# Optimization experiments

Hardware: AMD Instinct MI355X
Metric: run time of the kernel (lower is better)

Reference implementation:

```python
import jax, jax.numpy as jnp
import numpy as np
from jax import lax

EPS_IN = 1e-5  # torch InstanceNorm1d eps


def instance_norm(x, w, b):
    # x: (B, C, T); normalize over T per (B, C), biased variance
    mu = x.mean(axis=-1, keepdims=True)
    var = x.var(axis=-1, keepdims=True)
    return (x - mu) * lax.rsqrt(var + EPS_IN) * w[None, :, None] + b[None, :, None]


def conv1x1(x, w):
    # w: (O, I, 1)
    return jnp.einsum('oi,bit->bot', w[:, :, 0], x)


def setup_inputs() -> dict:
    key = jax.random.key(0)
    ks = jax.random.split(key, 16)
    B, C, T, NC = 32, 64, 2048, 4
    enc_dim = C * 3 * 4
    d = {
        'xb': jax.random.normal(ks[0], (B, 3, C, T), jnp.float32),
        'mu': jnp.linspace(-3.0, 3.0, 4),
        'sigma': jnp.full((4,), 2.0),
        'sconv1_w': jax.random.normal(ks[1], (128, enc_dim, 1)) * (1.0 / np.sqrt(enc_dim)),
        'in1_w': 1.0 + 0.1 * jax.random.normal(ks[2], (128,)),
        'in1_b': 0.1 * jax.random.normal(ks[3], (128,)),
        'sconv2_w': jax.random.normal(ks[4], (C, 128, 1)) * (1.0 / np.sqrt(128)),
        'in2_w': 1.0 + 0.1 * jax.random.normal(ks[5], (C,)),
        'in2_b': 0.1 * jax.random.normal(ks[6], (C,)),
        'tconv1_w': jax.random.normal(ks[7], (C, C, 15)) * (1.0 / np.sqrt(C * 15)),
        'in3_w': 1.0 + 0.1 * jax.random.normal(ks[8], (C,)),
        'in3_b': 0.1 * jax.random.normal(ks[9], (C,)),
        'tconv2_w': jax.random.normal(ks[10], (C, C, 1)) * (1.0 / np.sqrt(C)),
        'in4_w': 1.0 + 0.1 * jax.random.normal(ks[11], (C,)),
        'in4_b': 0.1 * jax.random.normal(ks[12], (C,)),
        'alpha': jnp.asarray(0.5),
        'gamma': jnp.asarray(0.5),
        'beta_logit': jnp.asarray(1.0),
        'fc_w': jax.random.normal(ks[13], (4, C)) * (1.0 / np.sqrt(C)),
        'fc_b': 0.1 * jax.random.normal(ks[14], (4,)),
    }
    return d


def reference(xb, mu, sigma, sconv1_w, in1_w, in1_b, sconv2_w, in2_w, in2_b,
              tconv1_w, in3_w, in3_b, tconv2_w, in4_w, in4_b,
              alpha, gamma, beta_logit, fc_w, fc_b):
    B, Ftypes, C, T = xb.shape
    V_BASE = 1.0
    Tp = T // 8

    # pooled curvature / tangent streams -> (T', B, C)
    curv_p = xb[:, 1].reshape(B, C, Tp, 8).mean(-1).transpose(2, 0, 1)
    tang_p = xb[:, 2].reshape(B, C, Tp, 8).mean(-1).transpose(2, 0, 1)

    # learnable population encoding: (B,3,C,T,4) -> (B, 3*C*4, T)
    enc = jnp.exp(-(xb[..., None] - mu) ** 2 / (2.0 * sigma ** 2 + 1e-6))
    x_enc = enc.transpose(0, 1, 2, 4, 3).reshape(B, Ftypes * C * 4, T)

    # spatial 1x1 convs + instance norm + relu
    h = jax.nn.relu(instance_norm(conv1x1(x_enc, sconv1_w), in1_w, in1_b))
    h = jax.nn.relu(instance_norm(conv1x1(h, sconv2_w), in2_w, in2_b))

    # temporal conv k=15 pad=7, 1x1 conv, avg pool 8
    h = lax.conv_general_dilated(h, tconv1_w, (1,), [(7, 7)],
                                 dimension_numbers=('NCH', 'OIH', 'NCH'))
    h = jax.nn.relu(instance_norm(h, in3_w, in3_b))
    h = jax.nn.relu(instance_norm(conv1x1(h, tconv2_w), in4_w, in4_b))
    h = h.reshape(B, C, Tp, 8).mean(-1)  # AvgPool1d(8)
    # dropout is identity in eval mode
    c = h.transpose(2, 0, 1)  # (T', B, C)

    # sequential GD-LIF recurrence over T' steps
    def step(m, inp):
        x_t, curv_t, tang_t = inp
        v_th = V_BASE + alpha * tang_t
        beta = jax.nn.sigmoid(beta_logit - gamma * curv_t)
        m_next = beta * m + x_t
        spike = (m_next - v_th > 0).astype(m_next.dtype)
        m_next = m_next - spike * v_th
        return m_next, spike

    m0 = jnp.zeros((B, C), xb.dtype)
    _, spikes = lax.scan(step, m0, (c, curv_p, tang_p))  # (T', B, C)

    attn = jax.nn.softmax(curv_p, axis=0)
    out_feat = jnp.sum(spikes * attn, axis=0)  # (B, C)
    return out_feat @ fc_w.T + fc_b
```

## Files before the change

### kernel.cpp

```cpp
#include <hip/hip_runtime.h>
#include <math.h>

#define TLEN 2048
#define TP 256

typedef double d4 __attribute__((ext_vector_type(4)));

__device__ __forceinline__ double block_reduce_sum_d(double v, double* sm) {
#pragma unroll
  for (int off = 32; off > 0; off >>= 1) v += __shfl_down(v, off, 64);
  int lane = threadIdx.x & 63, wid = threadIdx.x >> 6;
  __syncthreads();
  if (lane == 0) sm[wid] = v;
  __syncthreads();
  double r = sm[0] + sm[1] + sm[2] + sm[3];
  __syncthreads();
  return r;
}

__global__ void k_probe_f64(int* __restrict__ tbl) {
  int l = threadIdx.x;
  __shared__ int kaS[64], kbS[64];
  __shared__ int cnt[256];
  int rdv[4] = {-1, -1, -1, -1}, cdv[4] = {-1, -1, -1, -1};
  int mav = -1, nbv = -1;
  int okr = 1;
  int nrow = 0, ncol = 0;
  kaS[l] = -1; kbS[l] = -1;
  __syncthreads();

  for (int j = 0; j < 64; ++j) {
    double a = (l == j) ? 1.0 : 0.0;
    d4 acc = {0.0, 0.0, 0.0, 0.0};
    acc = __builtin_amdgcn_mfma_f64_16x16x4f64(a, 1.0, acc, 0, 0, 0);
    int mylab = -1;
#pragma unroll
    for (int v = 0; v < 4; ++v) if (acc[v] != 0.0 && rdv[v] >= 0) mylab = rdv[v];
#pragma unroll
    for (int off = 32; off >= 1; off >>= 1) {
      int o = __shfl_xor(mylab, off);
      mylab = mylab > o ? mylab : o;
    }
    int label = (mylab < 0) ? nrow : mylab;
    if (mylab < 0) nrow++;
    if (label >= 16) okr = 0;
#pragma unroll
    for (int v = 0; v < 4; ++v) if (acc[v] != 0.0) rdv[v] = label;
    if (l == j) mav = label;
  }

  for (int j = 0; j < 64; ++j) {
    double bb = (l == j) ? 1.0 : 0.0;
    d4 acc = {0.0, 0.0, 0.0, 0.0};
    acc = __builtin_amdgcn_mfma_f64_16x16x4f64(1.0, bb, acc, 0, 0, 0);
    int mylab = -1;
#pragma unroll
    for (int v = 0; v < 4; ++v) if (acc[v] != 0.0 && cdv[v] >= 0) mylab = cdv[v];
#pragma unroll
    for (int off = 32; off >= 1; off >>= 1) {
      int o = __shfl_xor(mylab, off);
      mylab = mylab > o ? mylab : o;
    }
    int label = (mylab < 0) ? ncol : mylab;
    if (mylab < 0) ncol++;
    if (label >= 16) okr = 0;
#pragma unroll
    for (int v = 0; v < 4; ++v) if (acc[v] != 0.0) cdv[v] = label;
    if (l == j) nbv = label;
  }

  unsigned long long row0 = __ballot(mav == 0);
  if (__popcll(row0) != 4) okr = 0;
  for (int i = 0; i < 4; ++i) {
    int rep = -1, idx = -1;
    for (int t = 0; t < 64; ++t)
      if ((row0 >> t) & 1ull) { if (++idx == i) { rep = t; break; } }
    double a = (l == rep) ? 1.0 : 0.0;
    double bb = (double)(l + 1);
    d4 acc = {0.0, 0.0, 0.0, 0.0};
    acc = __builtin_amdgcn_mfma_f64_16x16x4f64(a, bb, acc, 0, 0, 0);
#pragma unroll
    for (int v = 0; v < 4; ++v)
      if (rdv[v] == 0) {
        int jp = (int)(acc[v] + 0.5) - 1;
        if (jp >= 0 && jp < 64) kbS[jp] = i; else okr = 0;
      }
  }
  __syncthreads();
  int kbv = kbS[l];

  for (int i = 0; i < 4; ++i) {
    unsigned long long bm = __ballot(kbv == i);
    int rep = -1;
    if (bm != 0ull) { rep = 0; while (!((bm >> rep) & 1ull)) ++rep; }
    else okr = 0;
    int nc = (rep >= 0) ? __shfl(nbv, rep) : -2;
    double bb = (l == rep) ? 1.0 : 0.0;
    double aa = (double)(l + 1);
    d4 acc = {0.0, 0.0, 0.0, 0.0};
    acc = __builtin_amdgcn_mfma_f64_16x16x4f64(aa, bb, acc, 0, 0, 0);
#pragma unroll
    for (int v = 0; v < 4; ++v)
      if (cdv[v] == nc) {
        int jp = (int)(acc[v] + 0.5) - 1;
        if (jp >= 0 && jp < 64) kaS[jp] = i; else okr = 0;
      }
  }
  __syncthreads();
  int kav = kaS[l];

  if (nrow != 16 || ncol != 16) okr = 0;
  if (mav < 0 || mav > 15 || nbv < 0 || nbv > 15 ||
      kav < 0 || kav > 3 || kbv < 0 || kbv > 3) okr = 0;
#pragma unroll
  for (int v = 0; v < 4; ++v)
    if (rdv[v] < 0 || rdv[v] > 15 || cdv[v] < 0 || cdv[v] > 15) okr = 0;
  cnt[l] = 0; cnt[64 + l] = 0; cnt[128 + l] = 0; cnt[192 + l] = 0;
  __syncthreads();
  if (mav >= 0 && mav < 16 && kav >= 0 && kav < 4) atomicAdd(&cnt[mav * 4 + kav], 1);
  if (kbv >= 0 && kbv < 4 && nbv >= 0 && nbv < 16) atomicAdd(&cnt[64 + kbv * 16 + nbv], 1);
  __syncthreads();
  if (cnt[l] != 1 || cnt[64 + l] != 1) okr = 0;
  __syncthreads();
  cnt[l] = 0; cnt[64 + l] = 0; cnt[128 + l] = 0; cnt[192 + l] = 0;
  __syncthreads();
#pragma unroll
  for (int v = 0; v < 4; ++v)
    if (rdv[v] >= 0 && rdv[v] < 16 && cdv[v] >= 0 && cdv[v] < 16)
      atomicAdd(&cnt[rdv[v] * 16 + cdv[v]], 1);
  __syncthreads();
#pragma unroll
  for (int v = 0; v < 4; ++v) if (cnt[l * 4 + v] != 1) okr = 0;
  if (mav == 0) {
    int rank = (int)__popcll(row0 & ((1ull << l) - 1ull));
    if (kav != rank) okr = 0;
  }
  unsigned long long good = __ballot(okr != 0);
  tbl[l] = mav; tbl[64 + l] = kav; tbl[128 + l] = kbv; tbl[192 + l] = nbv;
#pragma unroll
  for (int v = 0; v < 4; ++v) {
    tbl[256 + l * 4 + v] = rdv[v];
    tbl[512 + l * 4 + v] = cdv[v];
  }
  if (l == 0) tbl[768] = (good == 0xFFFFFFFFFFFFFFFFull) ? 1 : 0;
}

__global__ void k_repack_w(const float* __restrict__ w, float* __restrict__ wT) {
  int idx = blockIdx.x * 256 + threadIdx.x;
  if (idx >= 64 * 64 * 15) return;
  int o = idx & 63, i = (idx >> 6) & 63, k = idx >> 12;
  wT[idx] = w[(o * 64 + i) * 15 + k];
}

template <typename T>
__global__ __launch_bounds__(256) void k_pool_ct(const float* __restrict__ xb,
                                                 T* __restrict__ curvp,
                                                 T* __restrict__ tangp) {
  int row = blockIdx.x;
  int b = row >> 6, c = row & 63;
  int tid = threadIdx.x;
  const float* s1 = xb + ((size_t)((b * 3 + 1) * 64 + c)) * TLEN + tid * 8;
  const float* s2 = xb + ((size_t)((b * 3 + 2) * 64 + c)) * TLEN + tid * 8;
  double p1 = 0.0, p2 = 0.0;
#pragma unroll
  for (int j = 0; j < 8; ++j) { p1 += (double)s1[j]; p2 += (double)s2[j]; }
  curvp[(size_t)row * TP + tid] = (T)(p1 * 0.125);
  tangp[(size_t)row * TP + tid] = (T)(p2 * 0.125);
}

template <typename T>
__global__ __launch_bounds__(256) void k_stats(const T* __restrict__ h,
                                               const float* __restrict__ gw,
                                               const float* __restrict__ gb,
                                               int chmask,
                                               double* __restrict__ sc,
                                               double* __restrict__ sh) {
  __shared__ double sm[4];
  int row = blockIdx.x, tid = threadIdx.x;
  int ch = row & chmask;
  const T* base = h + (size_t)row * TLEN + tid * 8;
  double v[8];
#pragma unroll
  for (int j = 0; j < 8; ++j) v[j] = (double)base[j];
  double s = 0.0;
#pragma unroll
  for (int j = 0; j < 8; ++j) s += v[j];
  double mean = block_reduce_sum_d(s, sm) * (1.0 / 2048.0);
  double sq = 0.0;
#pragma unroll
  for (int j = 0; j < 8; ++j) { double d = v[j] - mean; sq += d * d; }
  double var = block_reduce_sum_d(sq, sm) * (1.0 / 2048.0);
  double scale = (double)gw[ch] / sqrt(var + 1e-5);
  double shift = (double)gb[ch] - mean * scale;
  if (tid == 0) { sc[row] = scale; sh[row] = shift; }
}

template <typename T>
__global__ __launch_bounds__(256, 4) void k_enc1_mfma(const float* __restrict__ xb,
                                                      const float* __restrict__ w,
                                                      const float* __restrict__ mu,
                                                      const float* __restrict__ sigma,
                                                      T* __restrict__ h1,
                                                      const int* __restrict__ tbl) {
  if (tbl[768] == 0) return;
  __shared__ float AsT[32][132];
  __shared__ double Bs[32][68];
  __shared__ double smu[4], sinv[4];
  int b = blockIdx.x, t0 = blockIdx.y * 64, tid = threadIdx.x;
  int wv = tid >> 6, l = tid & 63;
  int t_ma = tbl[l], t_ka = tbl[64 + l], t_kb = tbl[128 + l], t_nb = tbl[192 + l];
  int t_rd[4], t_cd[4];
#pragma unroll
  for (int v = 0; v < 4; ++v) { t_rd[v] = tbl[256 + l * 4 + v]; t_cd[v] = tbl[512 + l * 4 + v]; }
  if (tid < 4) {
    smu[tid] = (double)mu[tid];
    double s = (double)sigma[tid];
    sinv[tid] = 1.0 / (2.0 * s * s + 1e-6);
  }
  d4 acc[2][4];
#pragma unroll
  for (int r = 0; r < 2; ++r)
#pragma unroll
    for (int c = 0; c < 4; ++c) acc[r][c] = (d4){0.0, 0.0, 0.0, 0.0};

  for (int kc = 0; kc < 24; ++kc) {
    int i0 = kc * 32;
    __syncthreads();
    {
      int idx = tid * 4;
#pragma unroll
      for (int rep = 0; rep < 4; ++rep) {
        int o = idx >> 5, ii = idx & 31;
        float4 v4 = *(const float4*)(w + (size_t)o * 768 + i0 + ii);
        AsT[ii][o] = v4.x; AsT[ii + 1][o] = v4.y; AsT[ii + 2][o] = v4.z; AsT[ii + 3][o] = v4.w;
        idx += 1024;
      }
    }
    {
      int f = i0 >> 8;
      int cb = (i0 >> 2) & 63;
      int c = tid >> 5, l2 = tid & 31;
      int t = 2 * l2;
      float2 x2 = *(const float2*)(xb + ((size_t)((b * 3 + f) * 64 + cb + c)) * TLEN + t0 + t);
      double xv0 = (double)x2.x, xv1 = (double)x2.y;
#pragma unroll
      for (int g = 0; g < 4; ++g) {
        double m = smu[g], inv = sinv[g];
        double d0 = xv0 - m, d1 = xv1 - m;
        double2 e = {exp(-d0 * d0 * inv), exp(-d1 * d1 * inv)};
        *(double2*)&Bs[c * 4 + g][t] = e;
      }
    }
    __syncthreads();
#pragma unroll
    for (int k4 = 0; k4 < 32; k4 += 4) {
      double aF0 = (double)AsT[k4 + t_ka][wv * 32 + t_ma];
      double aF1 = (double)AsT[k4 + t_ka][wv * 32 + 16 + t_ma];
      double bF[4];
#pragma unroll
      for (int c = 0; c < 4; ++c) bF[c] = Bs[k4 + t_kb][c * 16 + t_nb];
#pragma unroll
      for (int c = 0; c < 4; ++c) {
        acc[0][c] = __builtin_amdgcn_mfma_f64_16x16x4f64(aF0, bF[c], acc[0][c], 0, 0, 0);
        acc[1][c] = __builtin_amdgcn_mfma_f64_16x16x4f64(aF1, bF[c], acc[1][c], 0, 0, 0);
      }
    }
  }
#pragma unroll
  for (int r = 0; r < 2; ++r)
#pragma unroll
    for (int c = 0; c < 4; ++c)
#pragma unroll
      for (int v = 0; v < 4; ++v) {
        int o = wv * 32 + r * 16 + t_rd[v];
        h1[((size_t)(b * 128 + o)) * TLEN + t0 + c * 16 + t_cd[v]] = (T)acc[r][c][v];
      }
}

template <typename T>
__global__ __launch_bounds__(256, 4) void k_enc1_valu(const float* __restrict__ xb,
                                                      const float* __restrict__ w,
                                                      const float* __restrict__ mu,
                                                      const float* __restrict__ sigma,
                                                      T* __restrict__ h1,
                                                      const int* __restrict__ tbl) {
  if (tbl[768] != 0) return;
  __shared__ float AsT[32][132];
  __shared__ double Bs[32][64];
  __shared__ double smu[4], sinv[4];
  int b = blockIdx.x, t0 = blockIdx.y * 64, tid = threadIdx.x;
  if (tid < 4) {
    smu[tid] = (double)mu[tid];
    double s = (double)sigma[tid];
    sinv[tid] = 1.0 / (2.0 * s * s + 1e-6);
  }
  double acc[8][4] = {};
  int to = (tid >> 4) * 8, l = tid & 15;
  for (int kc = 0; kc < 24; ++kc) {
    int i0 = kc * 32;
    __syncthreads();
    {
      int idx = tid * 4;
#pragma unroll
      for (int rep = 0; rep < 4; ++rep) {
        int o = idx >> 5, ii = idx & 31;
        float4 v4 = *(const float4*)(w + (size_t)o * 768 + i0 + ii);
        AsT[ii][o] = v4.x; AsT[ii + 1][o] = v4.y; AsT[ii + 2][o] = v4.z; AsT[ii + 3][o] = v4.w;
        idx += 1024;
      }
    }
    {
      int f = i0 >> 8;
      int cb = (i0 >> 2) & 63;
      int c = tid >> 5, l2 = tid & 31;
      int t = 2 * l2;
      float2 x2 = *(const float2*)(xb + ((size_t)((b * 3 + f) * 64 + cb + c)) * TLEN + t0 + t);
      double xv0 = (double)x2.x, xv1 = (double)x2.y;
#pragma unroll
      for (int g = 0; g < 4; ++g) {
        double m = smu[g], inv = sinv[g];
        double d0 = xv0 - m, d1 = xv1 - m;
        double2 e = {exp(-d0 * d0 * inv), exp(-d1 * d1 * inv)};
        *(double2*)&Bs[c * 4 + g][t] = e;
      }
    }
    __syncthreads();
#pragma unroll
    for (int kk = 0; kk < 32; ++kk) {
      float4 a0 = *(const float4*)&AsT[kk][to];
      float4 a1 = *(const float4*)&AsT[kk][to + 4];
      double a[8] = {(double)a0.x, (double)a0.y, (double)a0.z, (double)a0.w,
                     (double)a1.x, (double)a1.y, (double)a1.z, (double)a1.w};
      double bb[4];
#pragma unroll
      for (int j = 0; j < 2; ++j) {
        double2 p = *(const double2*)&Bs[kk][2 * l + 32 * j];
        bb[2 * j] = p.x; bb[2 * j + 1] = p.y;
      }
#pragma unroll
      for (int q = 0; q < 8; ++q)
#pragma unroll
        for (int j = 0; j < 4; ++j) acc[q][j] += a[q] * bb[j];
    }
  }
#pragma unroll
  for (int q = 0; q < 8; ++q) {
    T* op = h1 + ((size_t)(b * 128 + to + q)) * TLEN + t0;
    op[2 * l]      = (T)acc[q][0];
    op[2 * l + 1]  = (T)acc[q][1];
    op[2 * l + 32] = (T)acc[q][2];
    op[2 * l + 33] = (T)acc[q][3];
  }
}

template <int K, typename T>
__global__ __launch_bounds__(256, 4) void k_conv1x1_mfma(const T* __restrict__ in,
                                                         const float* __restrict__ w,
                                                         const double* __restrict__ sc,
                                                         const double* __restrict__ sh,
                                                         T* __restrict__ out,
                                                         const int* __restrict__ tbl) {
  if (tbl[768] == 0) return;
  __shared__ float AsT[32][68];
  __shared__ double Bs[32][68];
  int b = blockIdx.x, t0 = blockIdx.y * 64, tid = threadIdx.x;
  int wv = tid >> 6, l = tid & 63;
  int t_ma = tbl[l], t_ka = tbl[64 + l], t_kb = tbl[128 + l], t_nb = tbl[192 + l];
  int t_rd[4], t_cd[4];
#pragma unroll
  for (int v = 0; v < 4; ++v) { t_rd[v] = tbl[256 + l * 4 + v]; t_cd[v] = tbl[512 + l * 4 + v]; }
  int o0 = wv * 16;
  d4 acc[4];
#pragma unroll
  for (int c = 0; c < 4; ++c) acc[c] = (d4){0.0, 0.0, 0.0, 0.0};
  for (int kc = 0; kc < K / 32; ++kc) {
    __syncthreads();
    {
      int idx = tid * 4;
#pragma unroll
      for (int rep = 0; rep < 2; ++rep) {
        int o = idx >> 5, ii = idx & 31;
        float4 v4 = *(const float4*)(w + (size_t)o * K + kc * 32 + ii);
        AsT[ii][o] = v4.x; AsT[ii + 1][o] = v4.y; AsT[ii + 2][o] = v4.z; AsT[ii + 3][o] = v4.w;
        idx += 1024;
      }
    }
    {
      int r = tid >> 3, l8 = tid & 7;
      int srow = b * K + kc * 32 + r;
      const T* gp = in + (size_t)srow * TLEN + t0;
      double s_ = sc[srow], h_ = sh[srow];
#pragma unroll
      for (int q = 0; q < 4; ++q) {
        int t = 2 * l8 + 16 * q;
        double2 v = {fmax((double)gp[t] * s_ + h_, 0.0),
                     fmax((double)gp[t + 1] * s_ + h_, 0.0)};
        *(double2*)&Bs[r][t] = v;
      }
    }
    __syncthreads();
#pragma unroll
    for (int k4 = 0; k4 < 32; k4 += 4) {
      double aF = (double)AsT[k4 + t_ka][o0 + t_ma];
#pragma unroll
      for (int c = 0; c < 4; ++c) {
        double bF = Bs[k4 + t_kb][c * 16 + t_nb];
        acc[c] = __builtin_amdgcn_mfma_f64_16x16x4f64(aF, bF, acc[c], 0, 0, 0);
      }
    }
  }
#pragma unroll
  for (int c = 0; c < 4; ++c)
#pragma unroll
    for (int v = 0; v < 4; ++v)
      out[((size_t)(b * 64 + o0 + t_rd[v])) * TLEN + t0 + c * 16 + t_cd[v]] = (T)acc[c][v];
}

template <int K, typename T>
__global__ __launch_bounds__(256, 4) void k_conv1x1_valu(const T* __restrict__ in,
                                                         const float* __restrict__ w,
                                                         const double* __restrict__ sc,
                                                         const double* __restrict__ sh,
                                                         T* __restrict__ out,
                                                         const int* __restrict__ tbl) {
  if (tbl[768] != 0) return;
  __shared__ float AsT[32][68];
  __shared__ double Bs[32][64];
  int b = blockIdx.x, t0 = blockIdx.y * 64, tid = threadIdx.x;
  double acc[4][4] = {};
  int to = (tid >> 4) * 4, l = tid & 15;
  for (int kc = 0; kc < K / 32; ++kc) {
    __syncthreads();
    {
      int idx = tid * 4;
#pragma unroll
      for (int rep = 0; rep < 2; ++rep) {
        int o = idx >> 5, ii = idx & 31;
        float4 v4 = *(const float4*)(w + (size_t)o * K + kc * 32 + ii);
        AsT[ii][o] = v4.x; AsT[ii + 1][o] = v4.y; AsT[ii + 2][o] = v4.z; AsT[ii + 3][o] = v4.w;
        idx += 1024;
      }
    }
    {
      int r = tid >> 3, l8 = tid & 7;
      int srow = b * K + kc * 32 + r;
      const T* gp = in + (size_t)srow * TLEN + t0;
      double s_ = sc[srow], h_ = sh[srow];
#pragma unroll
      for (int q = 0; q < 4; ++q) {
        int t = 2 * l8 + 16 * q;
        double2 v = {fmax((double)gp[t] * s_ + h_, 0.0),
                     fmax((double)gp[t + 1] * s_ + h_, 0.0)};
        *(double2*)&Bs[r][t] = v;
      }
    }
    __syncthreads();
#pragma unroll
    for (int kk = 0; kk < 32; ++kk) {
      float4 a4 = *(const float4*)&AsT[kk][to];
      double a0 = (double)a4.x, a1 = (double)a4.y, a2 = (double)a4.z, a3 = (double)a4.w;
      double bb[4];
#pragma unroll
      for (int j = 0; j < 2; ++j) {
        double2 p = *(const double2*)&Bs[kk][2 * l + 32 * j];
        bb[2 * j] = p.x; bb[2 * j + 1] = p.y;
      }
#pragma unroll
      for (int j = 0; j < 4; ++j) {
        acc[0][j] += a0 * bb[j];
        acc[1][j] += a1 * bb[j];
        acc[2][j] += a2 * bb[j];
        acc[3][j] += a3 * bb[j];
      }
    }
  }
#pragma unroll
  for (int q = 0; q < 4; ++q) {
    T* op = out + ((size_t)(b * 64 + to + q)) * TLEN + t0;
    op[2 * l]      = (T)acc[q][0];
    op[2 * l + 1]  = (T)acc[q][1];
    op[2 * l + 32] = (T)acc[q][2];
    op[2 * l + 33] = (T)acc[q][3];
  }
}

template <typename T>
__global__ __launch_bounds__(256, 2) void k_tconv1_mfma(const T* __restrict__ h2,
                                                        const float* __restrict__ wT,
                                                        const double* __restrict__ sc,
                                                        const double* __restrict__ sh,
                                                        T* __restrict__ h3,
                                                        const int* __restrict__ tbl) {
  if (tbl[768] == 0) return;
  __shared__ __align__(16) double In[64][80];
  __shared__ float Ws[8][15][64];
  int b = blockIdx.x, t0 = blockIdx.y * 64, tid = threadIdx.x;
  int wv = tid >> 6, l = tid & 63;
  int t_ma = tbl[l], t_ka = tbl[64 + l], t_kb = tbl[128 + l], t_nb = tbl[192 + l];
  int t_rd[4], t_cd[4];
#pragma unroll
  for (int v = 0; v < 4; ++v) { t_rd[v] = tbl[256 + l * 4 + v]; t_cd[v] = tbl[512 + l * 4 + v]; }
  int o0 = wv * 16;
  for (int idx = tid; idx < 64 * 78; idx += 256) {
    int i = idx / 78, x = idx - i * 78;
    int tg = t0 - 7 + x;
    int row = b * 64 + i;
    double v = 0.0;
    if (tg >= 0 && tg < TLEN)
      v = fmax((double)h2[(size_t)row * TLEN + tg] * sc[row] + sh[row], 0.0);
    In[i][x] = v;
  }
  d4 acc[4];
#pragma unroll
  for (int c = 0; c < 4; ++c) acc[c] = (d4){0.0, 0.0, 0.0, 0.0};
  for (int ic = 0; ic < 8; ++ic) {
    __syncthreads();
    for (int idx = tid; idx < 15 * 8 * 16; idx += 256) {
      int k = idx >> 7;
      int r = idx & 127;
      int ii = r >> 4, o4 = (r & 15) * 4;
      float4 v = *(const float4*)(wT + ((size_t)(k * 64 + ic * 8 + ii)) * 64 + o4);
      *(float4*)&Ws[ii][k][o4] = v;
    }
    __syncthreads();
#pragma unroll
    for (int k = 0; k < 15; ++k) {
#pragma unroll
      for (int kg = 0; kg < 2; ++kg) {
        double aF = (double)Ws[kg * 4 + t_ka][k][o0 + t_ma];
#pragma unroll
        for (int c = 0; c < 4; ++c) {
          double bF = In[ic * 8 + kg * 4 + t_kb][c * 16 + t_nb + k];
          acc[c] = __builtin_amdgcn_mfma_f64_16x16x4f64(aF, bF, acc[c], 0, 0, 0);
        }
      }
    }
  }
#pragma unroll
  for (int c = 0; c < 4; ++c)
#pragma unroll
    for (int v = 0; v < 4; ++v)
      h3[((size_t)(b * 64 + o0 + t_rd[v])) * TLEN + t0 + c * 16 + t_cd[v]] = (T)acc[c][v];
}

template <typename T>
__global__ __launch_bounds__(256) void k_tconv1_valu(const T* __restrict__ h2,
                                                     const float* __restrict__ wT,
                                                     const double* __restrict__ sc,
                                                     const double* __restrict__ sh,
                                                     T* __restrict__ h3,
                                                     const int* __restrict__ tbl) {
  if (tbl[768] != 0) return;
  __shared__ __align__(16) double In[64][80];
  __shared__ float Ws[8][15][64];
  int b = blockIdx.x, t0 = blockIdx.y * 64, tid = threadIdx.x;
  for (int idx = tid; idx < 64 * 78; idx += 256) {
    int i = idx / 78, x = idx - i * 78;
    int tg = t0 - 7 + x;
    int row = b * 64 + i;
    double v = 0.0;
    if (tg >= 0 && tg < TLEN)
      v = fmax((double)h2[(size_t)row * TLEN + tg] * sc[row] + sh[row], 0.0);
    In[i][x] = v;
  }
  double acc[4][4] = {};
  int og = (tid >> 4) * 4, tt2 = (tid & 15) * 4;
  for (int ic = 0; ic < 8; ++ic) {
    __syncthreads();
    for (int idx = tid; idx < 15 * 8 * 16; idx += 256) {
      int k = idx >> 7;
      int r = idx & 127;
      int ii = r >> 4, o4 = (r & 15) * 4;
      float4 v = *(const float4*)(wT + ((size_t)(k * 64 + ic * 8 + ii)) * 64 + o4);
      *(float4*)&Ws[ii][k][o4] = v;
    }
    __syncthreads();
#pragma unroll
    for (int ii = 0; ii < 8; ++ii) {
      int i = ic * 8 + ii;
      double r[18];
#pragma unroll
      for (int m = 0; m < 18; m += 2) {
        double2 p = *(const double2*)&In[i][tt2 + m];
        r[m] = p.x; r[m + 1] = p.y;
      }
#pragma unroll
      for (int k = 0; k < 15; ++k) {
        float4 w4 = *(const float4*)&Ws[ii][k][og];
        double w0 = (double)w4.x, w1 = (double)w4.y, w2 = (double)w4.z, w3 = (double)w4.w;
#pragma unroll
        for (int j = 0; j < 4; ++j) {
          double x = r[j + k];
          acc[0][j] += w0 * x;
          acc[1][j] += w1 * x;
          acc[2][j] += w2 * x;
          acc[3][j] += w3 * x;
        }
      }
    }
  }
#pragma unroll
  for (int q = 0; q < 4; ++q) {
    T* op = h3 + ((size_t)(b * 64 + og + q)) * TLEN + t0 + tt2;
#pragma unroll
    for (int j = 0; j < 4; ++j) op[j] = (T)acc[q][j];
  }
}

template <typename T>
__global__ __launch_bounds__(256) void k_in4_pool(const T* __restrict__ h,
                                                  const float* __restrict__ gw,
                                                  const float* __restrict__ gb,
                                                  T* __restrict__ cbuf) {
  __shared__ double sm[4];
  int row = blockIdx.x, tid = threadIdx.x;
  int ch = row & 63;
  const T* base = h + (size_t)row * TLEN + tid * 8;
  double v[8];
#pragma unroll
  for (int j = 0; j < 8; ++j) v[j] = (double)base[j];
  double s = 0.0;
#pragma unroll
  for (int j = 0; j < 8; ++j) s += v[j];
  double mean = block_reduce_sum_d(s, sm) * (1.0 / 2048.0);
  double sq = 0.0;
#pragma unroll
  for (int j = 0; j < 8; ++j) { double d = v[j] - mean; sq += d * d; }
  double var = block_reduce_sum_d(sq, sm) * (1.0 / 2048.0);
  double scale = (double)gw[ch] / sqrt(var + 1e-5);
  double shift = (double)gb[ch] - mean * scale;
  double p = 0.0;
#pragma unroll
  for (int j = 0; j < 8; ++j) p += fmax(v[j] * scale + shift, 0.0);
  cbuf[(size_t)row * TP + tid] = (T)(p * 0.125);
}

template <typename T>
__global__ __launch_bounds__(64) void k_scan(const T* __restrict__ cbuf,
                                             const T* __restrict__ curvp,
                                             const T* __restrict__ tangp,
                                             const float* __restrict__ alpha,
                                             const float* __restrict__ gamma,
                                             const float* __restrict__ betal,
                                             double* __restrict__ ofeat) {
  int id = blockIdx.x * 64 + threadIdx.x;
  double a = (double)alpha[0], g = (double)gamma[0], bl = (double)betal[0];
  const T* cu_p = curvp + (size_t)id * TP;
  const T* ta_p = tangp + (size_t)id * TP;
  const T* cb_p = cbuf + (size_t)id * TP;
  double mmax = -1e300, ssum = 0.0;
  for (int tp = 0; tp < TP; ++tp) {
    double v = (double)cu_p[tp];
    double nm = fmax(mmax, v);
    ssum = ssum * exp(mmax - nm) + exp(v - nm);
    mmax = nm;
  }
  double invs = 1.0 / ssum;
  double mem = 0.0, acc = 0.0;
  for (int tp = 0; tp < TP; ++tp) {
    double x = (double)cb_p[tp];
    double cu = (double)cu_p[tp];
    double ta = (double)ta_p[tp];
    double vth = 1.0 + a * ta;
    double beta = 1.0 / (1.0 + exp(g * cu - bl));
    mem = beta * mem + x;
    if (mem - vth > 0.0) {
      acc += exp(cu - mmax) * invs;
      mem -= vth;
    }
  }
  ofeat[id] = acc;
}

__global__ void k_fc(const double* __restrict__ ofeat, const float* __restrict__ fw,
                     const float* __restrict__ fb, float* __restrict__ out) {
  int tid = threadIdx.x;
  if (tid >= 128) return;
  int b = tid >> 2, j = tid & 3;
  double s = (double)fb[j];
#pragma unroll
  for (int c = 0; c < 64; ++c) s += ofeat[b * 64 + c] * (double)fw[j * 64 + c];
  out[b * 4 + j] = (float)s;
}

template <typename T>
static void run_all(void* const* d_in, float* out, char* wsb, hipStream_t stream) {
  const float* xb    = (const float*)d_in[0];
  const float* mu    = (const float*)d_in[1];
  const float* sigma = (const float*)d_in[2];
  const float* w1    = (const float*)d_in[3];
  const float* in1w  = (const float*)d_in[4];
  const float* in1b  = (const float*)d_in[5];
  const float* w2    = (const float*)d_in[6];
  const float* in2w  = (const float*)d_in[7];
  const float* in2b  = (const float*)d_in[8];
  const float* wt1   = (const float*)d_in[9];
  const float* in3w  = (const float*)d_in[10];
  const float* in3b  = (const float*)d_in[11];
  const float* w4    = (const float*)d_in[12];
  const float* in4w  = (const float*)d_in[13];
  const float* in4b  = (const float*)d_in[14];
  const float* alpha = (const float*)d_in[15];
  const float* gamma = (const float*)d_in[16];
  const float* betal = (const float*)d_in[17];
  const float* fcw   = (const float*)d_in[18];
  const float* fcb   = (const float*)d_in[19];

  size_t sT = sizeof(T);
  T* h1 = (T*)wsb;
  T* h2 = (T*)(wsb + (size_t)8388608 * sT);
  T* h3 = h1;
  T* h4 = h2;
  float* wT = (float*)(wsb + (size_t)12582912 * sT);
  char* p = wsb + (size_t)12582912 * sT + 245760;
  T* curvp = (T*)p;
  T* tangp = (T*)(p + (size_t)524288 * sT);
  T* cbuf  = (T*)(p + (size_t)2 * 524288 * sT);
  double* ofeat = (double*)(p + (size_t)3 * 524288 * sT);
  char* cb = (char*)cbuf;
  int* tbl = (int*)cb;
  double* sc1 = (double*)(cb + 16384);
  double* sh1 = sc1 + 4096;
  double* sc2 = sh1 + 4096;
  double* sh2 = sc2 + 2048;
  double* sc3 = sh2 + 2048;
  double* sh3 = sc3 + 2048;

  k_repack_w<<<dim3(240), dim3(256), 0, stream>>>(wt1, wT);
  k_pool_ct<T><<<dim3(2048), dim3(256), 0, stream>>>(xb, curvp, tangp);
  k_probe_f64<<<dim3(1), dim3(64), 0, stream>>>(tbl);
  k_enc1_mfma<T><<<dim3(32, 32), dim3(256), 0, stream>>>(xb, w1, mu, sigma, h1, tbl);
  k_enc1_valu<T><<<dim3(32, 32), dim3(256), 0, stream>>>(xb, w1, mu, sigma, h1, tbl);
  k_stats<T><<<dim3(4096), dim3(256), 0, stream>>>(h1, in1w, in1b, 127, sc1, sh1);
  k_conv1x1_mfma<128, T><<<dim3(32, 32), dim3(256), 0, stream>>>(h1, w2, sc1, sh1, h2, tbl);
  k_conv1x1_valu<128, T><<<dim3(32, 32), dim3(256), 0, stream>>>(h1, w2, sc1, sh1, h2, tbl);
  k_stats<T><<<dim3(2048), dim3(256), 0, stream>>>(h2, in2w, in2b, 63, sc2, sh2);
  k_tconv1_mfma<T><<<dim3(32, 32), dim3(256), 0, stream>>>(h2, wT, sc2, sh2, h3, tbl);
  k_tconv1_valu<T><<<dim3(32, 32), dim3(256), 0, stream>>>(h2, wT, sc2, sh2, h3, tbl);
  k_stats<T><<<dim3(2048), dim3(256), 0, stream>>>(h3, in3w, in3b, 63, sc3, sh3);
  k_conv1x1_mfma<64, T><<<dim3(32, 32), dim3(256), 0, stream>>>(h3, w4, sc3, sh3, h4, tbl);
  k_conv1x1_valu<64, T><<<dim3(32, 32), dim3(256), 0, stream>>>(h3, w4, sc3, sh3, h4, tbl);
  k_in4_pool<T><<<dim3(2048), dim3(256), 0, stream>>>(h4, in4w, in4b, cbuf);
  k_scan<T><<<dim3(32), dim3(64), 0, stream>>>(cbuf, curvp, tangp, alpha, gamma, betal, ofeat);
  k_fc<<<dim3(1), dim3(128), 0, stream>>>(ofeat, fcw, fcb, out);
}

extern "C" void kernel_launch(void* const* d_in, const int* in_sizes, int n_in,
                              void* d_out, int out_size, void* d_ws, size_t ws_size,
                              hipStream_t stream) {
  const size_t NEED64 = 113508352ull;
  if (ws_size >= NEED64)
    run_all<double>(d_in, (float*)d_out, (char*)d_ws, stream);
  else
    run_all<float>(d_in, (float*)d_out, (char*)d_ws, stream);
}
```

Before: 641.4 us.

## Shrink enc1 K-tile, split tconv1 across 8 waves, fuse scan softmax pass

The enc1 MFMA kernel halves its K-chunk (16 instead of 32) to cut shared memory and raises launch bounds to 8 blocks per CU so more blocks stay resident. The temporal conv kernel moves to 512 threads, with each wave computing half the time columns, so more waves share the same staged input. The scan kernel merges the online-softmax pass into the recurrence loop, rescaling the spike accumulator as the running max changes, so the curvature data is read once. The enc1 change doubles the number of block-wide barriers, and the scan changes the floating-point evaluation order slightly.

```diff
diff --git a/kernel.cpp b/kernel.cpp
--- a/kernel.cpp
+++ b/kernel.cpp
@@ -196,15 +196,15 @@
 }
 
 template <typename T>
-__global__ __launch_bounds__(256, 4) void k_enc1_mfma(const float* __restrict__ xb,
+__global__ __launch_bounds__(256, 8) void k_enc1_mfma(const float* __restrict__ xb,
                                                       const float* __restrict__ w,
                                                       const float* __restrict__ mu,
                                                       const float* __restrict__ sigma,
                                                       T* __restrict__ h1,
                                                       const int* __restrict__ tbl) {
   if (tbl[768] == 0) return;
-  __shared__ float AsT[32][132];
-  __shared__ double Bs[32][68];
+  __shared__ float AsT[16][132];
+  __shared__ double Bs[16][68];
   __shared__ double smu[4], sinv[4];
   int b = blockIdx.x, t0 = blockIdx.y * 64, tid = threadIdx.x;
   int wv = tid >> 6, l = tid & 63;
@@ -212,6 +212,7 @@
   int t_rd[4], t_cd[4];
 #pragma unroll
   for (int v = 0; v < 4; ++v) { t_rd[v] = tbl[256 + l * 4 + v]; t_cd[v] = tbl[512 + l * 4 + v]; }
+  int o0 = wv * 32;
   if (tid < 4) {
     smu[tid] = (double)mu[tid];
     double s = (double)sigma[tid];
@@ -223,14 +224,14 @@
 #pragma unroll
     for (int c = 0; c < 4; ++c) acc[r][c] = (d4){0.0, 0.0, 0.0, 0.0};
 
-  for (int kc = 0; kc < 24; ++kc) {
-    int i0 = kc * 32;
+  for (int kc = 0; kc < 48; ++kc) {
+    int i0 = kc * 16;
     __syncthreads();
     {
       int idx = tid * 4;
 #pragma unroll
-      for (int rep = 0; rep < 4; ++rep) {
-        int o = idx >> 5, ii = idx & 31;
+      for (int rep = 0; rep < 2; ++rep) {
+        int o = idx >> 4, ii = idx & 15;
         float4 v4 = *(const float4*)(w + (size_t)o * 768 + i0 + ii);
         AsT[ii][o] = v4.x; AsT[ii + 1][o] = v4.y; AsT[ii + 2][o] = v4.z; AsT[ii + 3][o] = v4.w;
         idx += 1024;
@@ -239,23 +240,21 @@
     {
       int f = i0 >> 8;
       int cb = (i0 >> 2) & 63;
-      int c = tid >> 5, l2 = tid & 31;
-      int t = 2 * l2;
-      float2 x2 = *(const float2*)(xb + ((size_t)((b * 3 + f) * 64 + cb + c)) * TLEN + t0 + t);
-      double xv0 = (double)x2.x, xv1 = (double)x2.y;
+      int c = tid >> 6, l2 = tid & 63;
+      float x1 = xb[((size_t)((b * 3 + f) * 64 + cb + c)) * TLEN + t0 + l2];
+      double xv = (double)x1;
 #pragma unroll
       for (int g = 0; g < 4; ++g) {
         double m = smu[g], inv = sinv[g];
-        double d0 = xv0 - m, d1 = xv1 - m;
-        double2 e = {exp(-d0 * d0 * inv), exp(-d1 * d1 * inv)};
-        *(double2*)&Bs[c * 4 + g][t] = e;
-      }
-    }
-    __syncthreads();
-#pragma unroll
-    for (int k4 = 0; k4 < 32; k4 += 4) {
-      double aF0 = (double)AsT[k4 + t_ka][wv * 32 + t_ma];
-      double aF1 = (double)AsT[k4 + t_ka][wv * 32 + 16 + t_ma];
+        double d0 = xv - m;
+        Bs[c * 4 + g][l2] = exp(-d0 * d0 * inv);
+      }
+    }
+    __syncthreads();
+#pragma unroll
+    for (int k4 = 0; k4 < 16; k4 += 4) {
+      double aF0 = (double)AsT[k4 + t_ka][o0 + t_ma];
+      double aF1 = (double)AsT[k4 + t_ka][o0 + 16 + t_ma];
       double bF[4];
 #pragma unroll
       for (int c = 0; c < 4; ++c) bF[c] = Bs[k4 + t_kb][c * 16 + t_nb];
@@ -272,7 +271,7 @@
     for (int c = 0; c < 4; ++c)
 #pragma unroll
       for (int v = 0; v < 4; ++v) {
-        int o = wv * 32 + r * 16 + t_rd[v];
+        int o = o0 + r * 16 + t_rd[v];
         h1[((size_t)(b * 128 + o)) * TLEN + t0 + c * 16 + t_cd[v]] = (T)acc[r][c][v];
       }
 }
@@ -485,7 +484,7 @@
 }
 
 template <typename T>
-__global__ __launch_bounds__(256, 2) void k_tconv1_mfma(const T* __restrict__ h2,
+__global__ __launch_bounds__(512, 4) void k_tconv1_mfma(const T* __restrict__ h2,
                                                         const float* __restrict__ wT,
                                                         const double* __restrict__ sc,
                                                         const double* __restrict__ sh,
@@ -500,8 +499,8 @@
   int t_rd[4], t_cd[4];
 #pragma unroll
   for (int v = 0; v < 4; ++v) { t_rd[v] = tbl[256 + l * 4 + v]; t_cd[v] = tbl[512 + l * 4 + v]; }
-  int o0 = wv * 16;
-  for (int idx = tid; idx < 64 * 78; idx += 256) {
+  int o0 = (wv >> 1) * 16, tq = (wv & 1) * 32;
+  for (int idx = tid; idx < 64 * 78; idx += 512) {
     int i = idx / 78, x = idx - i * 78;
     int tg = t0 - 7 + x;
     int row = b * 64 + i;
@@ -510,12 +509,12 @@
       v = fmax((double)h2[(size_t)row * TLEN + tg] * sc[row] + sh[row], 0.0);
     In[i][x] = v;
   }
-  d4 acc[4];
-#pragma unroll
-  for (int c = 0; c < 4; ++c) acc[c] = (d4){0.0, 0.0, 0.0, 0.0};
+  d4 acc[2];
+  acc[0] = (d4){0.0, 0.0, 0.0, 0.0};
+  acc[1] = (d4){0.0, 0.0, 0.0, 0.0};
   for (int ic = 0; ic < 8; ++ic) {
     __syncthreads();
-    for (int idx = tid; idx < 15 * 8 * 16; idx += 256) {
+    for (int idx = tid; idx < 15 * 8 * 16; idx += 512) {
       int k = idx >> 7;
       int r = idx & 127;
       int ii = r >> 4, o4 = (r & 15) * 4;
@@ -529,18 +528,18 @@
       for (int kg = 0; kg < 2; ++kg) {
         double aF = (double)Ws[kg * 4 + t_ka][k][o0 + t_ma];
 #pragma unroll
-        for (int c = 0; c < 4; ++c) {
-          double bF = In[ic * 8 + kg * 4 + t_kb][c * 16 + t_nb + k];
+        for (int c = 0; c < 2; ++c) {
+          double bF = In[ic * 8 + kg * 4 + t_kb][tq + c * 16 + t_nb + k];
           acc[c] = __builtin_amdgcn_mfma_f64_16x16x4f64(aF, bF, acc[c], 0, 0, 0);
         }
       }
     }
   }
 #pragma unroll
-  for (int c = 0; c < 4; ++c)
+  for (int c = 0; c < 2; ++c)
 #pragma unroll
     for (int v = 0; v < 4; ++v)
-      h3[((size_t)(b * 64 + o0 + t_rd[v])) * TLEN + t0 + c * 16 + t_cd[v]] = (T)acc[c][v];
+      h3[((size_t)(b * 64 + o0 + t_rd[v])) * TLEN + t0 + tq + c * 16 + t_cd[v]] = (T)acc[c][v];
 }
 
 template <typename T>
@@ -648,28 +647,26 @@
   const T* cu_p = curvp + (size_t)id * TP;
   const T* ta_p = tangp + (size_t)id * TP;
   const T* cb_p = cbuf + (size_t)id * TP;
-  double mmax = -1e300, ssum = 0.0;
+  double mmax = -1e300, ssum = 0.0, accs = 0.0, mem = 0.0;
   for (int tp = 0; tp < TP; ++tp) {
-    double v = (double)cu_p[tp];
-    double nm = fmax(mmax, v);
-    ssum = ssum * exp(mmax - nm) + exp(v - nm);
-    mmax = nm;
-  }
-  double invs = 1.0 / ssum;
-  double mem = 0.0, acc = 0.0;
-  for (int tp = 0; tp < TP; ++tp) {
-    double x = (double)cb_p[tp];
     double cu = (double)cu_p[tp];
     double ta = (double)ta_p[tp];
+    double x = (double)cb_p[tp];
+    double nm = fmax(mmax, cu);
+    double r = exp(mmax - nm);
+    double e = exp(cu - nm);
+    ssum = ssum * r + e;
+    accs = accs * r;
+    mmax = nm;
     double vth = 1.0 + a * ta;
     double beta = 1.0 / (1.0 + exp(g * cu - bl));
     mem = beta * mem + x;
     if (mem - vth > 0.0) {
-      acc += exp(cu - mmax) * invs;
+      accs += e;
       mem -= vth;
     }
   }
-  ofeat[id] = acc;
+  ofeat[id] = accs / ssum;
 }
 
 __global__ void k_fc(const double* __restrict__ ofeat, const float* __restrict__ fw,
@@ -735,7 +732,7 @@
   k_conv1x1_mfma<128, T><<<dim3(32, 32), dim3(256), 0, stream>>>(h1, w2, sc1, sh1, h2, tbl);
   k_conv1x1_valu<128, T><<<dim3(32, 32), dim3(256), 0, stream>>>(h1, w2, sc1, sh1, h2, tbl);
   k_stats<T><<<dim3(2048), dim3(256), 0, stream>>>(h2, in2w, in2b, 63, sc2, sh2);
-  k_tconv1_mfma<T><<<dim3(32, 32), dim3(256), 0, stream>>>(h2, wT, sc2, sh2, h3, tbl);
+  k_tconv1_mfma<T><<<dim3(32, 32), dim3(512), 0, stream>>>(h2, wT, sc2, sh2, h3, tbl);
   k_tconv1_valu<T><<<dim3(32, 32), dim3(256), 0, stream>>>(h2, wT, sc2, sh2, h3, tbl);
   k_stats<T><<<dim3(2048), dim3(256), 0, stream>>>(h3, in3w, in3b, 63, sc3, sh3);
   k_conv1x1_mfma<64, T><<<dim3(32, 32), dim3(256), 0, stream>>>(h3, w4, sc3, sh3, h4, tbl);
```

After: 2.325 ms. +262.4%, slower.
